# Performance work log

Hardware: AMD Instinct MI355X
Metric: run time of the kernel (lower is better)

The kernel has to match this reference:

```python
import jax, jax.numpy as jnp
import numpy as np

B, T, D, H, L = 256, 512, 64, 256, 3  # batch, seq, input, hidden, layers

def setup_inputs() -> dict:
    key = jax.random.key(0)
    ks = jax.random.split(key, 16)
    k = 1.0 / np.sqrt(H)
    u = lambda kk, shape: jax.random.uniform(kk, shape, jnp.float32, -k, k)
    return {
        'x': jax.random.normal(ks[0], (B, T, D), jnp.float32),
        # layer 0 (input size D), 2 directions, PyTorch gate order i,f,g,o
        'Wih0': u(ks[1], (2, 4 * H, D)),
        'Whh0': u(ks[2], (2, 4 * H, H)),
        'bih0': u(ks[3], (2, 4 * H)),
        'bhh0': u(ks[4], (2, 4 * H)),
        # layers 1..L-1 (input size 2H from bidirectional concat)
        'Wih': u(ks[5], (L - 1, 2, 4 * H, 2 * H)),
        'Whh': u(ks[6], (L - 1, 2, 4 * H, H)),
        'bih': u(ks[7], (L - 1, 2, 4 * H)),
        'bhh': u(ks[8], (L - 1, 2, 4 * H)),
        'fc1_w': u(ks[9], (H, 2 * H)),
        'fc1_b': u(ks[10], (H,)),
        'fc2_w': u(ks[11], (1, H)),
        'fc2_b': u(ks[12], (1,)),
    }

def _run_dir(xs, wih, whh, bias, reverse):
    # xs: [T,B,Din]; precompute input-to-gate GEMM for all timesteps
    gx = jnp.einsum('tbd,gd->tbg', xs, wih) + bias  # [T,B,4H]
    h0 = jnp.zeros((xs.shape[1], whh.shape[1]), xs.dtype)
    def step(carry, g):
        h, c = carry
        z = g + h @ whh.T
        i, f, gg, o = jnp.split(z, 4, axis=-1)
        c = jax.nn.sigmoid(f) * c + jax.nn.sigmoid(i) * jnp.tanh(gg)
        h = jax.nn.sigmoid(o) * jnp.tanh(c)
        return (h, c), h
    (hT, _), hs = jax.lax.scan(step, (h0, h0), gx, reverse=reverse)
    return hs, hT

def reference(x, Wih0, Whh0, bih0, bhh0, Wih, Whh, bih, bhh, fc1_w, fc1_b, fc2_w, fc2_b):
    xs = jnp.transpose(x, (1, 0, 2))  # [T,B,D]
    hs_f, hT_f = _run_dir(xs, Wih0[0], Whh0[0], bih0[0] + bhh0[0], False)
    hs_b, hT_b = _run_dir(xs, Wih0[1], Whh0[1], bih0[1] + bhh0[1], True)
    xs = jnp.concatenate([hs_f, hs_b], axis=-1)
    for l in range(Wih.shape[0]):
        hs_f, hT_f = _run_dir(xs, Wih[l, 0], Whh[l, 0], bih[l, 0] + bhh[l, 0], False)
        hs_b, hT_b = _run_dir(xs, Wih[l, 1], Whh[l, 1], bih[l, 1] + bhh[l, 1], True)
        xs = jnp.concatenate([hs_f, hs_b], axis=-1)
    hidden = jnp.concatenate([hT_f, hT_b], axis=-1)  # [B,2H]
    h1 = jax.nn.relu(hidden @ fc1_w.T + fc1_b)
    return jax.nn.sigmoid(h1 @ fc2_w.T + fc2_b)  # [B,1]
```

## Files before the change

### kernel.cpp

```cpp
#include <hip/hip_runtime.h>

typedef unsigned short u16;
typedef short bf16x8 __attribute__((ext_vector_type(8)));
typedef float f32x4 __attribute__((ext_vector_type(4)));
typedef u16 u16x4 __attribute__((ext_vector_type(4)));

__device__ __forceinline__ u16 f2bf(float f) {
  union { float f; unsigned u; } v; v.f = f;
  unsigned r = v.u + 0x7fffu + ((v.u >> 16) & 1u);
  return (u16)(r >> 16);
}
__device__ __forceinline__ float bf2f(u16 h) {
  union { unsigned u; float f; } v; v.u = ((unsigned)h) << 16; return v.f;
}
__device__ __forceinline__ int perm(int p) {
  return (((p & 127) >> 5) << 8) | ((p >> 7) << 5) | (p & 31);
}
__device__ __forceinline__ float sigf(float x) {
  return __builtin_amdgcn_rcpf(1.f + __expf(-x));
}
__device__ __forceinline__ float tanhf_(float x) {
  return 1.f - 2.f * __builtin_amdgcn_rcpf(__expf(2.f * x) + 1.f);
}
__device__ __forceinline__ void gload_lds16(const void* g, void* l) {
  __builtin_amdgcn_global_load_lds((const __attribute__((address_space(1))) void*)g,
                                   (__attribute__((address_space(3))) void*)l, 16, 0, 0);
}

__global__ void sentinel(float* out, int n) {
  int i = blockIdx.x * 64 + threadIdx.x;
  if (i < n) out[i] = 1.0e6f;
}

__global__ __launch_bounds__(256) void prep_w(
    const float* __restrict__ Wih0, const float* __restrict__ Whh0,
    const float* __restrict__ bih0, const float* __restrict__ bhh0,
    const float* __restrict__ Wih,  const float* __restrict__ Whh,
    const float* __restrict__ bih,  const float* __restrict__ bhh,
    u16* __restrict__ wih0p, u16* __restrict__ wihp,
    u16* __restrict__ whhp, float* __restrict__ biasp)
{
  int idx = blockIdx.x * 256 + threadIdx.x;
  if (idx < 131072) {
    int j = idx;
    int d = j >> 16, p = (j >> 6) & 1023, k = j & 63;
    wih0p[j] = f2bf(Wih0[((size_t)d * 1024 + perm(p)) * 64 + k]);
  } else if (idx < 2228224) {
    int j = idx - 131072;
    int ld = j >> 19, p = (j >> 9) & 1023, k = j & 511;
    wihp[j] = f2bf(Wih[((size_t)ld * 1024 + perm(p)) * 512 + k]);
  } else if (idx < 3801088) {
    int j = idx - 2228224;
    int g = j >> 18, p = (j >> 8) & 1023, k = j & 255;
    int l = g >> 1, d = g & 1;
    float v = (l == 0) ? Whh0[((size_t)d * 1024 + perm(p)) * 256 + k]
                       : Whh[((size_t)((l - 1) * 2 + d) * 1024 + perm(p)) * 256 + k];
    whhp[j] = f2bf(v);
  } else if (idx < 3807232) {
    int j = idx - 3801088;
    int g = j >> 10, p = j & 1023;
    int l = g >> 1, d = g & 1, pp = perm(p);
    float v = (l == 0) ? (bih0[d * 1024 + pp] + bhh0[d * 1024 + pp])
                       : (bih[((l - 1) * 2 + d) * 1024 + pp] + bhh[((l - 1) * 2 + d) * 1024 + pp]);
    biasp[j] = v;
  }
}

__global__ __launch_bounds__(256) void prep_x(
    const float* __restrict__ x, u16* __restrict__ xT, int b0, int lgB)
{
  int idx = blockIdx.x * 256 + threadIdx.x;
  int k = idx & 63;
  int bl = (idx >> 6) & ((1 << lgB) - 1);
  int t = idx >> (6 + lgB);
  xT[idx] = f2bf(x[((size_t)(b0 + bl) * 512 + t) * 64 + k]);
}

__global__ __launch_bounds__(256) void gx_gemm(
    const u16* __restrict__ A, int K,
    const u16* __restrict__ W, const float* __restrict__ bias,
    u16* __restrict__ gx, int tb2, int sgn, int lgB)
{
  __shared__ u16 aL[128 * 32];
  __shared__ u16 wL[128 * 32];
  int bid = blockIdx.x;
  int ntile = bid & 7, mtile = bid >> 3;
  int tid = threadIdx.x;
  int lane = tid & 63, wid = tid >> 6;
  int l15 = lane & 15, l4 = lane >> 4;
  int mh = wid >> 1, nh = wid & 1;
  int Bmask = (1 << lgB) - 1;
  f32x4 acc[4][4] = {};
  int nk = K >> 5;
  for (int bk = 0; bk < nk; ++bk) {
    __syncthreads();
    #pragma unroll
    for (int iss = 0; iss < 2; ++iss) {
      int s = iss * 256 + tid;
      int r = s >> 2, g = s & 3;
      int sg = g ^ (r & 3);
      int m = mtile * 128 + r;
      int trow = tb2 + sgn * (m >> lgB);
      int bl = m & Bmask;
      gload_lds16(A + (((size_t)trow << lgB) + bl) * K + (bk * 32 + sg * 8),
                  &aL[(size_t)(iss * 256 + wid * 64) * 8]);
      int wn = ntile * 128 + r;
      gload_lds16(W + (size_t)wn * K + (bk * 32 + sg * 8),
                  &wL[(size_t)(iss * 256 + wid * 64) * 8]);
    }
    __syncthreads();
    bf16x8 af[4], bf[4];
    #pragma unroll
    for (int i = 0; i < 4; ++i) {
      int ar = mh * 64 + i * 16 + l15;
      af[i] = *(const bf16x8*)&aL[(ar * 4 + (l4 ^ (ar & 3))) * 8];
      int br = nh * 64 + i * 16 + l15;
      bf[i] = *(const bf16x8*)&wL[(br * 4 + (l4 ^ (br & 3))) * 8];
    }
    #pragma unroll
    for (int i = 0; i < 4; ++i)
      #pragma unroll
      for (int j = 0; j < 4; ++j)
        acc[i][j] = __builtin_amdgcn_mfma_f32_16x16x32_bf16(af[i], bf[j], acc[i][j], 0, 0, 0);
  }
  #pragma unroll
  for (int i = 0; i < 4; ++i) {
    #pragma unroll
    for (int j = 0; j < 4; ++j) {
      int gn = ntile * 128 + nh * 64 + j * 16 + l15;
      float bj = bias[gn];
      #pragma unroll
      for (int r = 0; r < 4; ++r) {
        int gm = mtile * 128 + mh * 64 + i * 16 + l4 * 4 + r;
        gx[(size_t)gm * 1024 + gn] = f2bf(acc[i][j][r] + bj);
      }
    }
  }
}

__global__ __launch_bounds__(256, 1) void recur(
    const u16* __restrict__ whhL, const u16* __restrict__ gxf, const u16* __restrict__ gxb,
    u16* __restrict__ xsOut, float* __restrict__ cg, int* __restrict__ flags,
    int chunk, int TC, int lgB, int lgNBT)
{
  int bid = blockIdx.x;
  int gs = bid >> (1 + lgNBT);
  int rest = bid & ((2 << lgNBT) - 1);
  int d = rest >> lgNBT;
  int bt = rest & ((1 << lgNBT) - 1);
  int tid = threadIdx.x;
  int lane = tid & 63, w = tid >> 6;
  int l15 = lane & 15, l4 = lane >> 4;

  bf16x8 bfr[2][8];
  {
    const u16* wp = whhL + (size_t)d * 262144 + (size_t)(gs * 128 + w * 32) * 256;
    #pragma unroll
    for (int nt = 0; nt < 2; ++nt)
      #pragma unroll
      for (int kk = 0; kk < 8; ++kk)
        bfr[nt][kk] = *(const bf16x8*)&wp[(size_t)(nt * 16 + l15) * 256 + kk * 32 + l4 * 8];
  }

  int q0 = tid * 4;
  int bloc = q0 >> 5, hc0 = q0 & 31;
  int bglob = bt * 32 + bloc;
  float creg[4];
  if (chunk == 0) {
    creg[0] = 0.f; creg[1] = 0.f; creg[2] = 0.f; creg[3] = 0.f;
  } else {
    const float* cp = cg + (((size_t)d << lgB) + bglob) * 256 + gs * 32 + hc0;
    creg[0] = cp[0]; creg[1] = cp[1]; creg[2] = cp[2]; creg[3] = cp[3];
  }

  __shared__ float zl[32][132];
  int tbase = chunk * TC;
  int flgBase = (d * (1 << lgNBT) + bt) * 8;
  const u16* gxp = d ? gxb : gxf;

  for (int s = 0; s < TC; ++s) {
    int t  = d ? (511 - tbase - s) : (tbase + s);
    int tp = d ? (t + 1) : (t - 1);
    bool first = (chunk == 0 && s == 0);

    float gxv[2][2][4];
    #pragma unroll
    for (int mt = 0; mt < 2; ++mt)
      #pragma unroll
      for (int nt = 0; nt < 2; ++nt) {
        int col = gs * 128 + w * 32 + nt * 16 + l15;
        #pragma unroll
        for (int r = 0; r < 4; ++r) {
          int row = bt * 32 + mt * 16 + l4 * 4 + r;
          gxv[mt][nt][r] = bf2f(gxp[(((size_t)s << lgB) + row) * 1024 + col]);
        }
      }

    if (s > 0) {
      if (tid < 8)
        while (__hip_atomic_load(&flags[flgBase + tid], __ATOMIC_RELAXED,
                                 __HIP_MEMORY_SCOPE_AGENT) < s) {}
      __syncthreads();
      __builtin_amdgcn_fence(__ATOMIC_ACQUIRE, "agent");
    }

    f32x4 acc[2][2] = {};
    if (!first) {
      const u16* hp = xsOut + (((size_t)tp << lgB) + bt * 32) * 512 + d * 256;
      bf16x8 afr[2][8];
      #pragma unroll
      for (int mt = 0; mt < 2; ++mt)
        #pragma unroll
        for (int kk = 0; kk < 8; ++kk)
          afr[mt][kk] = *(const bf16x8*)&hp[(size_t)(mt * 16 + l15) * 512 + kk * 32 + l4 * 8];
      #pragma unroll
      for (int kk = 0; kk < 8; ++kk)
        #pragma unroll
        for (int mt = 0; mt < 2; ++mt)
          #pragma unroll
          for (int nt = 0; nt < 2; ++nt)
            acc[mt][nt] = __builtin_amdgcn_mfma_f32_16x16x32_bf16(afr[mt][kk], bfr[nt][kk], acc[mt][nt], 0, 0, 0);
    }

    #pragma unroll
    for (int mt = 0; mt < 2; ++mt)
      #pragma unroll
      for (int nt = 0; nt < 2; ++nt)
        #pragma unroll
        for (int r = 0; r < 4; ++r)
          zl[mt * 16 + l4 * 4 + r][w * 32 + nt * 16 + l15] = acc[mt][nt][r] + gxv[mt][nt][r];
    __syncthreads();

    f32x4 vi = *(const f32x4*)&zl[bloc][hc0];
    f32x4 vf = *(const f32x4*)&zl[bloc][32 + hc0];
    f32x4 vg = *(const f32x4*)&zl[bloc][64 + hc0];
    f32x4 vo = *(const f32x4*)&zl[bloc][96 + hc0];
    float hnew[4];
    #pragma unroll
    for (int j = 0; j < 4; ++j) {
      float c = sigf(vf[j]) * creg[j] + sigf(vi[j]) * tanhf_(vg[j]);
      creg[j] = c;
      hnew[j] = sigf(vo[j]) * tanhf_(c);
    }
    {
      size_t ho = (((size_t)t << lgB) + bglob) * 512 + d * 256 + gs * 32 + hc0;
      unsigned lo = (unsigned)f2bf(hnew[0]) | ((unsigned)f2bf(hnew[1]) << 16);
      unsigned hi = (unsigned)f2bf(hnew[2]) | ((unsigned)f2bf(hnew[3]) << 16);
      unsigned* dst = (unsigned*)(xsOut + ho);
      __hip_atomic_store(dst, lo, __ATOMIC_RELAXED, __HIP_MEMORY_SCOPE_AGENT);
      __hip_atomic_store(dst + 1, hi, __ATOMIC_RELAXED, __HIP_MEMORY_SCOPE_AGENT);
    }
    if (s == TC - 1) {
      float* cp = cg + (((size_t)d << lgB) + bglob) * 256 + gs * 32 + hc0;
      cp[0] = creg[0]; cp[1] = creg[1]; cp[2] = creg[2]; cp[3] = creg[3];
    }
    __syncthreads();
    if (tid == 0)
      __hip_atomic_store(&flags[flgBase + gs], s + 1, __ATOMIC_RELAXED, __HIP_MEMORY_SCOPE_AGENT);
  }
}

__global__ __launch_bounds__(256) void head(
    const u16* __restrict__ xs, const float* __restrict__ w1, const float* __restrict__ b1,
    const float* __restrict__ w2, const float* __restrict__ b2, float* __restrict__ out,
    int b0, int lgB)
{
  int b = blockIdx.x, tid = threadIdx.x;
  __shared__ float hid[512];
  __shared__ float red[4];
  for (int j = tid; j < 512; j += 256) {
    float v = (j < 256) ? bf2f(xs[(((size_t)511 << lgB) + b) * 512 + j])
                        : bf2f(xs[((size_t)b) * 512 + j]);
    hid[j] = v;
  }
  __syncthreads();
  float acc = b1[tid];
  const float* wr = w1 + (size_t)tid * 512;
  for (int k = 0; k < 512; ++k) acc = fmaf(hid[k], wr[k], acc);
  float h1 = fmaxf(acc, 0.f);
  float p = h1 * w2[tid];
  #pragma unroll
  for (int off = 32; off > 0; off >>= 1) p += __shfl_down(p, off, 64);
  if ((tid & 63) == 0) red[tid >> 6] = p;
  __syncthreads();
  if (tid == 0) {
    float sum = red[0] + red[1] + red[2] + red[3] + b2[0];
    out[b0 + b] = 1.f / (1.f + __expf(-sum));
  }
}

extern "C" void kernel_launch(void* const* d_in, const int* in_sizes, int n_in,
                              void* d_out, int out_size, void* d_ws, size_t ws_size,
                              hipStream_t stream)
{
  const float* x    = (const float*)d_in[0];
  const float* Wih0 = (const float*)d_in[1];
  const float* Whh0 = (const float*)d_in[2];
  const float* bih0 = (const float*)d_in[3];
  const float* bhh0 = (const float*)d_in[4];
  const float* Wih  = (const float*)d_in[5];
  const float* Whh  = (const float*)d_in[6];
  const float* bih  = (const float*)d_in[7];
  const float* bhh  = (const float*)d_in[8];
  const float* fc1w = (const float*)d_in[9];
  const float* fc1b = (const float*)d_in[10];
  const float* fc2w = (const float*)d_in[11];
  const float* fc2b = (const float*)d_in[12];
  float* out = (float*)d_out;

  const size_t SZ_WIH0 = 262144, SZ_WIH = 4194304, SZ_WHH = 3145728,
               SZ_BIAS = 24576, SZ_FLAGS = 196608;
  const size_t fixed = SZ_WIH0 + SZ_WIH + SZ_WHH + SZ_BIAS + SZ_FLAGS;
  const int cand[7][2] = {{256,64},{256,32},{256,16},{128,64},{128,32},{64,32},{32,32}};
  int Bg = 0, TC = 0;
  for (int i = 0; i < 7; ++i) {
    size_t bg = cand[i][0], tc = cand[i][1];
    size_t need = fixed + 2048 * bg  + 4096 * tc * bg
                + 2 * 524288 * bg ;
    if (need <= ws_size) { Bg = cand[i][0]; TC = cand[i][1]; break; }
  }
  if (!Bg) {
    sentinel<<<dim3((out_size + 63) / 64), dim3(64), 0, stream>>>(out, out_size);
    return;
  }
  int lgB = 31 - __builtin_clz((unsigned)Bg);
  int lgNBT = lgB - 5;
  int NBT = Bg >> 5;
  int NC = 512 / TC;
  int NGB = 256 / Bg;

  char* ws = (char*)d_ws;
  size_t off = 0;
  u16* wih0p   = (u16*)(ws + off); off += SZ_WIH0;
  u16* wihp    = (u16*)(ws + off); off += SZ_WIH;
  u16* whhp    = (u16*)(ws + off); off += SZ_WHH;
  float* biasp = (float*)(ws + off); off += SZ_BIAS;
  int* flags   = (int*)(ws + off); off += SZ_FLAGS;
  float* cgb   = (float*)(ws + off); off += 2048 * (size_t)Bg;
  u16* gxf     = (u16*)(ws + off); off += 2048 * (size_t)TC * Bg;
  u16* gxb     = (u16*)(ws + off); off += 2048 * (size_t)TC * Bg;
  u16* bufA    = (u16*)(ws + off); off += 524288 * (size_t)Bg;
  u16* bufB    = (u16*)(ws + off); off += 524288 * (size_t)Bg;
  u16* xT      = bufB;

  hipMemsetAsync(flags, 0, SZ_FLAGS, stream);
  prep_w<<<dim3(14872), dim3(256), 0, stream>>>(Wih0, Whh0, bih0, bhh0, Wih, Whh, bih, bhh,
                                                wih0p, wihp, whhp, biasp);
  for (int g = 0; g < NGB; ++g) {
    int b0 = g * Bg;
    prep_x<<<dim3(128 * Bg), dim3(256), 0, stream>>>(x, xT, b0, lgB);
    for (int l = 0; l < 3; ++l) {
      const u16* Ain = (l == 0) ? xT : ((l == 1) ? bufA : bufB);
      u16* Bout = (l == 1) ? bufB : bufA;
      int K = l ? 512 : 64;
      int mtiles = (TC * Bg) >> 7;
      for (int c = 0; c < NC; ++c) {
        for (int dct = 0; dct < 2; ++dct) {
          const u16* Wd = (l == 0) ? (wih0p + (size_t)dct * 65536)
                                   : (wihp + (size_t)((l - 1) * 2 + dct) * 524288);
          const float* bd = biasp + (size_t)(l * 2 + dct) * 1024;
          u16* gxd = dct ? gxb : gxf;
          int tb2 = dct ? (511 - c * TC) : (c * TC);
          int sgn = dct ? -1 : 1;
          gx_gemm<<<dim3(mtiles * 8), dim3(256), 0, stream>>>(Ain, K, Wd, bd, gxd, tb2, sgn, lgB);
        }
        int region = (g * 3 + l) * NC + c;
        recur<<<dim3(16 * NBT), dim3(256), 0, stream>>>(whhp + (size_t)l * 524288, gxf, gxb,
                                                        Bout, cgb, flags + region * 128,
                                                        c, TC, lgB, lgNBT);
      }
    }
    head<<<dim3(Bg), dim3(256), 0, stream>>>(bufA, fc1w, fc1b, fc2w, fc2b, out, b0, lgB);
  }
}
```

Measured before the change: 18.85 ms.

## Overlap next-chunk input GEMM with recurrence in a fused double-buffered kernel

Replaces the separate per-chunk gx_gemm launches plus recur launch with one fused kernel. Extra blocks in that kernel compute the input-gate GEMM for the next time chunk into a double buffer while the recurrence blocks process the current chunk. The gx output moves to an MFMA-fragment-tiled layout so recurrence blocks can load each fragment with one 8-byte read, and the h store is merged into a single 64-bit atomic. Flags now hold a running absolute step count per layer instead of per-chunk regions, and the chunk-length candidates shrink. The cost is that GEMM blocks compete with the latency-bound recurrence blocks for CUs and bandwidth.

```diff
diff --git a/kernel.cpp b/kernel.cpp
--- a/kernel.cpp
+++ b/kernel.cpp
@@ -76,16 +76,12 @@
   xT[idx] = f2bf(x[((size_t)(b0 + bl) * 512 + t) * 64 + k]);
 }
 
-__global__ __launch_bounds__(256) void gx_gemm(
-    const u16* __restrict__ A, int K,
-    const u16* __restrict__ W, const float* __restrict__ bias,
-    u16* __restrict__ gx, int tb2, int sgn, int lgB)
-{
-  __shared__ u16 aL[128 * 32];
-  __shared__ u16 wL[128 * 32];
-  int bid = blockIdx.x;
-  int ntile = bid & 7, mtile = bid >> 3;
-  int tid = threadIdx.x;
+__device__ __forceinline__ void gemm_tile(
+    const u16* __restrict__ A, int K, const u16* __restrict__ W,
+    const float* __restrict__ bias, u16* __restrict__ gxO,
+    int tb2, int sgn, int lgB, int mtile, int ntile,
+    u16* aL, u16* wL, int tid)
+{
   int lane = tid & 63, wid = tid >> 6;
   int l15 = lane & 15, l4 = lane >> 4;
   int mh = wid >> 1, nh = wid & 1;
@@ -127,28 +123,74 @@
   for (int i = 0; i < 4; ++i) {
     #pragma unroll
     for (int j = 0; j < 4; ++j) {
-      int gn = ntile * 128 + nh * 64 + j * 16 + l15;
-      float bj = bias[gn];
-      #pragma unroll
-      for (int r = 0; r < 4; ++r) {
-        int gm = mtile * 128 + mh * 64 + i * 16 + l4 * 4 + r;
-        gx[(size_t)gm * 1024 + gn] = f2bf(acc[i][j][r] + bj);
-      }
-    }
-  }
-}
-
-__global__ __launch_bounds__(256, 1) void recur(
-    const u16* __restrict__ whhL, const u16* __restrict__ gxf, const u16* __restrict__ gxb,
+      int row16 = mtile * 8 + mh * 4 + i;
+      int col16 = ntile * 8 + nh * 4 + j;
+      float bj = bias[col16 * 16 + l15];
+      u16x4 o;
+      #pragma unroll
+      for (int r = 0; r < 4; ++r) o[r] = f2bf(acc[i][j][r] + bj);
+      *(u16x4*)&gxO[(((size_t)row16 * 64 + col16) * 64 + lane) * 4] = o;
+    }
+  }
+}
+
+__global__ __launch_bounds__(256) void gx_chunk(
+    const u16* __restrict__ A, int K,
+    const u16* __restrict__ Wf, const u16* __restrict__ Wb,
+    const float* __restrict__ biasA,
+    u16* __restrict__ gxWf, u16* __restrict__ gxWb,
+    int cn, int TC, int lgB)
+{
+  __shared__ u16 aL[4096];
+  __shared__ u16 wL[4096];
+  int mtilesC = (TC << lgB) >> 7;
+  int halfT = mtilesC * 8;
+  int tt = blockIdx.x;
+  int dct = tt >= halfT;
+  int tl = dct ? tt - halfT : tt;
+  gemm_tile(A, K, dct ? Wb : Wf, biasA + dct * 1024, dct ? gxWb : gxWf,
+            dct ? (511 - cn * TC) : (cn * TC), dct ? -1 : 1,
+            lgB, tl >> 3, tl & 7, aL, wL, (int)threadIdx.x);
+}
+
+__global__ __launch_bounds__(256, 2) void fused(
+    const u16* __restrict__ whhL,
+    const u16* __restrict__ gxRf, const u16* __restrict__ gxRb,
+    u16* __restrict__ gxWf, u16* __restrict__ gxWb,
+    const u16* __restrict__ A, int K,
+    const u16* __restrict__ Wf, const u16* __restrict__ Wb,
+    const float* __restrict__ biasA,
     u16* __restrict__ xsOut, float* __restrict__ cg, int* __restrict__ flags,
-    int chunk, int TC, int lgB, int lgNBT)
-{
+    int chunk, int TC, int lgB, int lgNBT, int hasGemm)
+{
+  __shared__ union {
+    struct { u16 aL[4096]; u16 wL[4096]; } g;
+    float zl[32][132];
+  } sm;
   int bid = blockIdx.x;
+  int NR = 16 << lgNBT;
+  int tid = threadIdx.x;
+
+  if (bid >= NR) {
+    if (!hasGemm) return;
+    int NG = gridDim.x - NR;
+    int mtilesC = (TC << lgB) >> 7;
+    int halfT = mtilesC * 8;
+    int cn = chunk + 1;
+    for (int tt = bid - NR; tt < 2 * halfT; tt += NG) {
+      int dct = tt >= halfT;
+      int tl = dct ? tt - halfT : tt;
+      gemm_tile(A, K, dct ? Wb : Wf, biasA + dct * 1024, dct ? gxWb : gxWf,
+                dct ? (511 - cn * TC) : (cn * TC), dct ? -1 : 1,
+                lgB, tl >> 3, tl & 7, sm.g.aL, sm.g.wL, tid);
+    }
+    return;
+  }
+
   int gs = bid >> (1 + lgNBT);
   int rest = bid & ((2 << lgNBT) - 1);
   int d = rest >> lgNBT;
   int bt = rest & ((1 << lgNBT) - 1);
-  int tid = threadIdx.x;
   int lane = tid & 63, w = tid >> 6;
   int l15 = lane & 15, l4 = lane >> 4;
 
@@ -173,33 +215,31 @@
     creg[0] = cp[0]; creg[1] = cp[1]; creg[2] = cp[2]; creg[3] = cp[3];
   }
 
-  __shared__ float zl[32][132];
   int tbase = chunk * TC;
-  int flgBase = (d * (1 << lgNBT) + bt) * 8;
-  const u16* gxp = d ? gxb : gxf;
+  int flgBase = ((d << lgNBT) + bt) * 8;
+  const u16* gxp = d ? gxRb : gxRf;
+  int rstride = 1 << (lgB - 4);
 
   for (int s = 0; s < TC; ++s) {
     int t  = d ? (511 - tbase - s) : (tbase + s);
     int tp = d ? (t + 1) : (t - 1);
     bool first = (chunk == 0 && s == 0);
 
-    float gxv[2][2][4];
+    unsigned long long gq[2][2];
     #pragma unroll
     for (int mt = 0; mt < 2; ++mt)
       #pragma unroll
       for (int nt = 0; nt < 2; ++nt) {
-        int col = gs * 128 + w * 32 + nt * 16 + l15;
-        #pragma unroll
-        for (int r = 0; r < 4; ++r) {
-          int row = bt * 32 + mt * 16 + l4 * 4 + r;
-          gxv[mt][nt][r] = bf2f(gxp[(((size_t)s << lgB) + row) * 1024 + col]);
-        }
+        int row16 = s * rstride + bt * 2 + mt;
+        int col16 = gs * 8 + w * 2 + nt;
+        gq[mt][nt] = *(const unsigned long long*)&gxp[(((size_t)row16 * 64 + col16) * 64 + lane) * 4];
       }
+    asm volatile("" :: "v"(gq[0][0]), "v"(gq[0][1]), "v"(gq[1][0]), "v"(gq[1][1]));
 
     if (s > 0) {
       if (tid < 8)
         while (__hip_atomic_load(&flags[flgBase + tid], __ATOMIC_RELAXED,
-                                 __HIP_MEMORY_SCOPE_AGENT) < s) {}
+                                 __HIP_MEMORY_SCOPE_AGENT) < tbase + s) {}
       __syncthreads();
       __builtin_amdgcn_fence(__ATOMIC_ACQUIRE, "agent");
     }
@@ -228,13 +268,14 @@
       for (int nt = 0; nt < 2; ++nt)
         #pragma unroll
         for (int r = 0; r < 4; ++r)
-          zl[mt * 16 + l4 * 4 + r][w * 32 + nt * 16 + l15] = acc[mt][nt][r] + gxv[mt][nt][r];
+          sm.zl[mt * 16 + l4 * 4 + r][w * 32 + nt * 16 + l15] =
+              acc[mt][nt][r] + bf2f((u16)(gq[mt][nt] >> (16 * r)));
     __syncthreads();
 
-    f32x4 vi = *(const f32x4*)&zl[bloc][hc0];
-    f32x4 vf = *(const f32x4*)&zl[bloc][32 + hc0];
-    f32x4 vg = *(const f32x4*)&zl[bloc][64 + hc0];
-    f32x4 vo = *(const f32x4*)&zl[bloc][96 + hc0];
+    f32x4 vi = *(const f32x4*)&sm.zl[bloc][hc0];
+    f32x4 vf = *(const f32x4*)&sm.zl[bloc][32 + hc0];
+    f32x4 vg = *(const f32x4*)&sm.zl[bloc][64 + hc0];
+    f32x4 vo = *(const f32x4*)&sm.zl[bloc][96 + hc0];
     float hnew[4];
     #pragma unroll
     for (int j = 0; j < 4; ++j) {
@@ -246,9 +287,9 @@
       size_t ho = (((size_t)t << lgB) + bglob) * 512 + d * 256 + gs * 32 + hc0;
       unsigned lo = (unsigned)f2bf(hnew[0]) | ((unsigned)f2bf(hnew[1]) << 16);
       unsigned hi = (unsigned)f2bf(hnew[2]) | ((unsigned)f2bf(hnew[3]) << 16);
-      unsigned* dst = (unsigned*)(xsOut + ho);
-      __hip_atomic_store(dst, lo, __ATOMIC_RELAXED, __HIP_MEMORY_SCOPE_AGENT);
-      __hip_atomic_store(dst + 1, hi, __ATOMIC_RELAXED, __HIP_MEMORY_SCOPE_AGENT);
+      unsigned long long hv = (unsigned long long)lo | ((unsigned long long)hi << 32);
+      __hip_atomic_store((unsigned long long*)(xsOut + ho), hv,
+                         __ATOMIC_RELAXED, __HIP_MEMORY_SCOPE_AGENT);
     }
     if (s == TC - 1) {
       float* cp = cg + (((size_t)d << lgB) + bglob) * 256 + gs * 32 + hc0;
@@ -256,7 +297,8 @@
     }
     __syncthreads();
     if (tid == 0)
-      __hip_atomic_store(&flags[flgBase + gs], s + 1, __ATOMIC_RELAXED, __HIP_MEMORY_SCOPE_AGENT);
+      __hip_atomic_store(&flags[flgBase + gs], tbase + s + 1,
+                         __ATOMIC_RELAXED, __HIP_MEMORY_SCOPE_AGENT);
   }
 }
 
@@ -309,13 +351,13 @@
   float* out = (float*)d_out;
 
   const size_t SZ_WIH0 = 262144, SZ_WIH = 4194304, SZ_WHH = 3145728,
-               SZ_BIAS = 24576, SZ_FLAGS = 196608;
+               SZ_BIAS = 24576, SZ_FLAGS = 16384;
   const size_t fixed = SZ_WIH0 + SZ_WIH + SZ_WHH + SZ_BIAS + SZ_FLAGS;
-  const int cand[7][2] = {{256,64},{256,32},{256,16},{128,64},{128,32},{64,32},{32,32}};
+  const int cand[6][2] = {{256,32},{256,16},{128,32},{128,16},{64,16},{32,16}};
   int Bg = 0, TC = 0;
-  for (int i = 0; i < 7; ++i) {
+  for (int i = 0; i < 6; ++i) {
     size_t bg = cand[i][0], tc = cand[i][1];
-    size_t need = fixed + 2048 * bg  + 4096 * tc * bg
+    size_t need = fixed + 2048 * bg  + 4 * 2048 * tc * bg
                 + 2 * 524288 * bg ;
     if (need <= ws_size) { Bg = cand[i][0]; TC = cand[i][1]; break; }
   }
@@ -328,6 +370,10 @@
   int NBT = Bg >> 5;
   int NC = 512 / TC;
   int NGB = 256 / Bg;
+  int NR = 16 * NBT;
+  int NGRID = NR + 896;
+  size_t SZGX = 2048 * (size_t)TC * Bg;
+  int halfT = ((TC << lgB) >> 7) * 8;
 
   char* ws = (char*)d_ws;
   size_t off = 0;
@@ -337,8 +383,11 @@
   float* biasp = (float*)(ws + off); off += SZ_BIAS;
   int* flags   = (int*)(ws + off); off += SZ_FLAGS;
   float* cgb   = (float*)(ws + off); off += 2048 * (size_t)Bg;
-  u16* gxf     = (u16*)(ws + off); off += 2048 * (size_t)TC * Bg;
-  u16* gxb     = (u16*)(ws + off); off += 2048 * (size_t)TC * Bg;
+  u16* gxbuf[2][2];
+  gxbuf[0][0] = (u16*)(ws + off); off += SZGX;
+  gxbuf[0][1] = (u16*)(ws + off); off += SZGX;
+  gxbuf[1][0] = (u16*)(ws + off); off += SZGX;
+  gxbuf[1][1] = (u16*)(ws + off); off += SZGX;
   u16* bufA    = (u16*)(ws + off); off += 524288 * (size_t)Bg;
   u16* bufB    = (u16*)(ws + off); off += 524288 * (size_t)Bg;
   u16* xT      = bufB;
@@ -353,21 +402,19 @@
       const u16* Ain = (l == 0) ? xT : ((l == 1) ? bufA : bufB);
       u16* Bout = (l == 1) ? bufB : bufA;
       int K = l ? 512 : 64;
-      int mtiles = (TC * Bg) >> 7;
+      const u16* Wf = (l == 0) ? wih0p : (wihp + (size_t)((l - 1) * 2) * 524288);
+      const u16* Wb = (l == 0) ? (wih0p + 65536) : (wihp + (size_t)((l - 1) * 2 + 1) * 524288);
+      const float* biasA = biasp + (size_t)(l * 2) * 1024;
+      const u16* whh_l = whhp + (size_t)l * 524288;
+      int* flg = flags + (g * 3 + l) * 128;
+      gx_chunk<<<dim3(2 * halfT), dim3(256), 0, stream>>>(Ain, K, Wf, Wb, biasA,
+                                                          gxbuf[0][0], gxbuf[0][1], 0, TC, lgB);
       for (int c = 0; c < NC; ++c) {
-        for (int dct = 0; dct < 2; ++dct) {
-          const u16* Wd = (l == 0) ? (wih0p + (size_t)dct * 65536)
-                                   : (wihp + (size_t)((l - 1) * 2 + dct) * 524288);
-          const float* bd = biasp + (size_t)(l * 2 + dct) * 1024;
-          u16* gxd = dct ? gxb : gxf;
-          int tb2 = dct ? (511 - c * TC) : (c * TC);
-          int sgn = dct ? -1 : 1;
-          gx_gemm<<<dim3(mtiles * 8), dim3(256), 0, stream>>>(Ain, K, Wd, bd, gxd, tb2, sgn, lgB);
-        }
-        int region = (g * 3 + l) * NC + c;
-        recur<<<dim3(16 * NBT), dim3(256), 0, stream>>>(whhp + (size_t)l * 524288, gxf, gxb,
-                                                        Bout, cgb, flags + region * 128,
-                                                        c, TC, lgB, lgNBT);
+        int cur = c & 1, nxt = cur ^ 1;
+        int hasg = (c + 1 < NC) ? 1 : 0;
+        fused<<<dim3(NGRID), dim3(256), 0, stream>>>(
+            whh_l, gxbuf[cur][0], gxbuf[cur][1], gxbuf[nxt][0], gxbuf[nxt][1],
+            Ain, K, Wf, Wb, biasA, Bout, cgb, flg, c, TC, lgB, lgNBT, hasg);
       }
     }
     head<<<dim3(Bg), dim3(256), 0, stream>>>(bufA, fc1w, fc1b, fc2w, fc2b, out, b0, lgB);
```

Result: slower. 19.79 ms (+5.0%).
